# Kernel tuning notes

Measured on AMD Instinct MI355X. Metric: run time of the kernel, lower is better.

## Reference

```python
import jax, jax.numpy as jnp
import numpy as np

B, S, D, H, DFF = 4, 1024, 1024, 16, 4096
DK = D // H
EPS = 1e-9


def _layernorm(x, alpha, bias):
    # Faithful to source: torch.std is unbiased (ddof=1), eps added to std.
    mean = jnp.mean(x, axis=-1, keepdims=True)
    xc = x - mean
    std = jnp.sqrt(jnp.sum(xc * xc, axis=-1, keepdims=True) / (x.shape[-1] - 1))
    return alpha * xc / (std + EPS) + bias


def _mha(x, wq_w, wq_b, wo_w, wo_b):
    # Source bug preserved: w_q is used for q, k, AND v projections.
    p = (x @ wq_w + wq_b).reshape(B, S, H, DK).transpose(0, 2, 1, 3)  # [B,H,S,DK]
    scores = jnp.einsum('bhqd,bhkd->bhqk', p, p) / jnp.sqrt(jnp.asarray(DK, x.dtype))
    attn = jax.nn.softmax(scores, axis=-1)
    out = jnp.einsum('bhqk,bhkd->bhqd', attn, p)
    out = out.transpose(0, 2, 1, 3).reshape(B, S, D)
    return out @ wo_w + wo_b


def _ffn(x, w1, b1, w2, b2):
    return jax.nn.relu(x @ w1 + b1) @ w2 + b2


def setup_inputs() -> dict:
    key = jax.random.key(0)
    ks = jax.random.split(key, 8)
    sc = 0.02
    return {
        'x': jax.random.normal(ks[0], (B, S, D), jnp.float32),
        'wq_w': sc * jax.random.normal(ks[1], (D, D), jnp.float32),
        'wq_b': jnp.zeros((D,), jnp.float32),
        'wo_w': sc * jax.random.normal(ks[2], (D, D), jnp.float32),
        'wo_b': jnp.zeros((D,), jnp.float32),
        'ff1_w': sc * jax.random.normal(ks[3], (D, DFF), jnp.float32),
        'ff1_b': jnp.zeros((DFF,), jnp.float32),
        'ff2_w': sc * jax.random.normal(ks[4], (DFF, D), jnp.float32),
        'ff2_b': jnp.zeros((D,), jnp.float32),
        'alpha1': jnp.ones((1,), jnp.float32), 'bias1': jnp.zeros((1,), jnp.float32),
        'alpha2': jnp.ones((1,), jnp.float32), 'bias2': jnp.zeros((1,), jnp.float32),
        'alpha3': jnp.ones((1,), jnp.float32), 'bias3': jnp.zeros((1,), jnp.float32),
    }


def reference(x, wq_w, wq_b, wo_w, wo_b, ff1_w, ff1_b, ff2_w, ff2_b,
              alpha1, bias1, alpha2, bias2, alpha3, bias3):
    h1 = x + _mha(_layernorm(x, alpha1, bias1), wq_w, wq_b, wo_w, wo_b)
    h2 = h1 + _ffn(_layernorm(h1, alpha2, bias2), ff1_w, ff1_b, ff2_w, ff2_b)
    return _layernorm(h2, alpha3, bias3)
```

## Files before the change

kernel.cpp:

```cpp
#include <hip/hip_runtime.h>

typedef short short8 __attribute__((ext_vector_type(8)));
typedef float f32x4 __attribute__((ext_vector_type(4)));
typedef unsigned short u16x4 __attribute__((ext_vector_type(4)));

#define DEV static __device__ __forceinline__

DEV float b2f(unsigned short u) { return __uint_as_float(((unsigned)u) << 16); }
DEV unsigned short f2b(float f) {
    unsigned u = __float_as_uint(f);
    u += 0x7FFFu + ((u >> 16) & 1u);
    return (unsigned short)(u >> 16);
}
DEV float wred_sum(float v) {
#pragma unroll
    for (int o = 32; o; o >>= 1) v += __shfl_xor(v, o);
    return v;
}

DEV void gld_lds16(const unsigned short* g, unsigned short* l) {
    __builtin_amdgcn_global_load_lds((const __attribute__((address_space(1))) void*)g,
                                     (__attribute__((address_space(3))) void*)l, 16, 0, 0);
}

template <bool OUT_BF16>
__global__ __launch_bounds__(256) void ln_kernel(const float* __restrict__ in,
                                                 void* __restrict__ out_v,
                                                 const float* __restrict__ alpha_p,
                                                 const float* __restrict__ bias_p) {
    __shared__ float redA[4], redB[4];
    const int row = blockIdx.x;
    const int t = threadIdx.x;
    const int lane = t & 63, w = t >> 6;

    f32x4 xv = *(const f32x4*)&in[(size_t)row * 1024 + t * 4];

    float s = wred_sum(xv[0] + xv[1] + xv[2] + xv[3]);
    if (lane == 0) redA[w] = s;
    __syncthreads();
    float mean = (redA[0] + redA[1] + redA[2] + redA[3]) * (1.0f / 1024.0f);

    float d0 = xv[0] - mean, d1 = xv[1] - mean, d2 = xv[2] - mean, d3 = xv[3] - mean;
    float ss = wred_sum(d0 * d0 + d1 * d1 + d2 * d2 + d3 * d3);
    if (lane == 0) redB[w] = ss;
    __syncthreads();
    float var = (redB[0] + redB[1] + redB[2] + redB[3]) * (1.0f / 1023.0f);
    float denom = sqrtf(var) + 1e-9f;
    float inv = alpha_p[0] / denom;
    float bias = bias_p[0];

    if (OUT_BF16) {
        u16x4 o;
        o[0] = f2b(d0 * inv + bias);
        o[1] = f2b(d1 * inv + bias);
        o[2] = f2b(d2 * inv + bias);
        o[3] = f2b(d3 * inv + bias);
        *(u16x4*)&((unsigned short*)out_v)[(size_t)row * 1024 + t * 4] = o;
    } else {
        f32x4 o;
        o[0] = d0 * inv + bias;
        o[1] = d1 * inv + bias;
        o[2] = d2 * inv + bias;
        o[3] = d3 * inv + bias;
        *(f32x4*)&((float*)out_v)[(size_t)row * 1024 + t * 4] = o;
    }
}

__global__ __launch_bounds__(256) void transpose_cast_kernel(const float* __restrict__ in,
                                                             unsigned short* __restrict__ out,
                                                             int R, int C) {
    __shared__ unsigned short tile[32][33];
    const int c0 = blockIdx.x * 32, r0 = blockIdx.y * 32;
    const int x = threadIdx.x, y0 = threadIdx.y;
#pragma unroll
    for (int yy = y0; yy < 32; yy += 8) tile[yy][x] = f2b(in[(size_t)(r0 + yy) * C + c0 + x]);
    __syncthreads();
#pragma unroll
    for (int yy = y0; yy < 32; yy += 8) out[(size_t)(c0 + yy) * R + r0 + x] = tile[x][yy];
}

__global__ __launch_bounds__(256) void transpose_bf16_batch(const unsigned short* __restrict__ in,
                                                            unsigned short* __restrict__ out) {
    __shared__ unsigned short tile[32][33];
    const int b = blockIdx.z;
    const int d0 = blockIdx.x * 32, s0 = blockIdx.y * 32;
    const unsigned short* I = in + (size_t)b * 1024 * 1024;
    unsigned short* O = out + (size_t)b * 1024 * 1024;
    const int x = threadIdx.x, y0 = threadIdx.y;
#pragma unroll
    for (int yy = y0; yy < 32; yy += 8) tile[yy][x] = I[(size_t)(s0 + yy) * 1024 + d0 + x];
    __syncthreads();
#pragma unroll
    for (int yy = y0; yy < 32; yy += 8) O[(size_t)(d0 + yy) * 1024 + s0 + x] = tile[x][yy];
}

template <int BM, int BN, bool RELU, bool RES, bool OUT_BF16>
__global__ __launch_bounds__(256) void gemm2(const unsigned short* __restrict__ A,
                                             const unsigned short* __restrict__ Bt,
                                             const float* __restrict__ bias,
                                             const float* __restrict__ res,
                                             void* __restrict__ C_v,
                                             int M, int N, int K) {
    constexpr int WM = BM / 2, WN = BN / 2;
    constexpr int FM = WM / 16, FN = WN / 16;
    __shared__ __align__(16) unsigned short As[BM * 64];
    __shared__ __align__(16) unsigned short Bs[BN * 64];

    const int t = threadIdx.x;
    const int lane = t & 63, w = t >> 6;
    const int wr = w >> 1, wc = w & 1;
    const int lr = lane & 15, g = lane >> 4;

    const int nwg = gridDim.x;
    const int cpx = nwg >> 3;
    const int wg = blockIdx.x;
    const int swz = (wg & 7) * cpx + (wg >> 3);
    const int NB = N / BN;
    const int m0 = (swz / NB) * BM, n0 = (swz % NB) * BN;

    f32x4 acc[FM][FN];
#pragma unroll
    for (int i = 0; i < FM; ++i)
#pragma unroll
        for (int j = 0; j < FN; ++j) acc[i][j] = (f32x4)0.0f;

    for (int k0 = 0; k0 < K; k0 += 64) {
        __syncthreads();
#pragma unroll
        for (int i = 0; i < BM / 32; ++i) {
            int id = i * 256 + t;
            int row = id >> 3, ch = id & 7;
            gld_lds16(&A[(size_t)(m0 + row) * K + k0 + ((ch ^ (row & 7)) * 8)],
                      &As[(size_t)(i * 256 + (t & ~63)) * 8]);
        }
#pragma unroll
        for (int i = 0; i < BN / 32; ++i) {
            int id = i * 256 + t;
            int row = id >> 3, ch = id & 7;
            gld_lds16(&Bt[(size_t)(n0 + row) * K + k0 + ((ch ^ (row & 7)) * 8)],
                      &Bs[(size_t)(i * 256 + (t & ~63)) * 8]);
        }
        __syncthreads();

        short8 af[FM][2], bfr[FN][2];
#pragma unroll
        for (int mi = 0; mi < FM; ++mi) {
            int row = wr * WM + mi * 16 + lr;
#pragma unroll
            for (int ks = 0; ks < 2; ++ks) {
                int ch = (ks * 4 + g) ^ (row & 7);
                af[mi][ks] = *(const short8*)&As[row * 64 + ch * 8];
            }
        }
#pragma unroll
        for (int ni = 0; ni < FN; ++ni) {
            int row = wc * WN + ni * 16 + lr;
#pragma unroll
            for (int ks = 0; ks < 2; ++ks) {
                int ch = (ks * 4 + g) ^ (row & 7);
                bfr[ni][ks] = *(const short8*)&Bs[row * 64 + ch * 8];
            }
        }
#pragma unroll
        for (int ks = 0; ks < 2; ++ks)
#pragma unroll
            for (int mi = 0; mi < FM; ++mi)
#pragma unroll
                for (int ni = 0; ni < FN; ++ni)
                    acc[mi][ni] = __builtin_amdgcn_mfma_f32_16x16x32_bf16(af[mi][ks], bfr[ni][ks], acc[mi][ni], 0, 0, 0);
    }

    const int lg = g;
#pragma unroll
    for (int ni = 0; ni < FN; ++ni) {
        int col = n0 + wc * WN + ni * 16 + lr;
        float bv = bias[col];
#pragma unroll
        for (int mi = 0; mi < FM; ++mi) {
            int row0 = m0 + wr * WM + mi * 16 + lg * 4;
#pragma unroll
            for (int i = 0; i < 4; ++i) {
                int row = row0 + i;
                float x = acc[mi][ni][i] + bv;
                if (RES) x += res[(size_t)row * N + col];
                if (RELU) x = fmaxf(x, 0.0f);
                if (OUT_BF16)
                    ((unsigned short*)C_v)[(size_t)row * N + col] = f2b(x);
                else
                    ((float*)C_v)[(size_t)row * N + col] = x;
            }
        }
    }
}

__global__ __launch_bounds__(256) void attn_mfma_kernel(const unsigned short* __restrict__ p,
                                                        const unsigned short* __restrict__ pT,
                                                        unsigned short* __restrict__ out) {
    __shared__ __align__(16) unsigned short Ks[64 * 64];
    __shared__ __align__(16) unsigned short Vt[64 * 64];
    __shared__ __align__(16) unsigned short Ps[4 * 16 * 64];

    const int t = threadIdx.x;
    const int lane = t & 63, w = t >> 6;
    const int lr = lane & 15, g = lane >> 4;
    const int qblk = blockIdx.x;
    const int bh = blockIdx.y;
    const int b = bh >> 4, h = bh & 15;

    const unsigned short* Pm = p + (size_t)b * (1024 * 1024) + h * 64;
    const unsigned short* PT = pT + (size_t)b * (1024 * 1024) + (size_t)(h * 64) * 1024;

    const int q0 = qblk * 64 + w * 16;
    short8 qa0 = *(const short8*)&Pm[(size_t)(q0 + lr) * 1024 + g * 8];
    short8 qa1 = *(const short8*)&Pm[(size_t)(q0 + lr) * 1024 + 32 + g * 8];

    f32x4 acc[4];
#pragma unroll
    for (int i = 0; i < 4; ++i) acc[i] = (f32x4)0.0f;
    float mrow[4] = {-1e30f, -1e30f, -1e30f, -1e30f};
    float lsum[4] = {0.f, 0.f, 0.f, 0.f};

    unsigned short* Pw = &Ps[w * 16 * 64];

    for (int kt = 0; kt < 16; ++kt) {
        const int key0 = kt * 64;
        __syncthreads();
#pragma unroll
        for (int i = 0; i < 2; ++i) {
            int id = t + i * 256;
            int row = id >> 3, ch = (id & 7) * 8;
            int sw = ch ^ ((row & 7) << 3);
            short8 kv = *(const short8*)&Pm[(size_t)(key0 + row) * 1024 + ch];
            *(short8*)&Ks[row * 64 + sw] = kv;
            short8 vv = *(const short8*)&PT[(size_t)row * 1024 + key0 + ch];
            *(short8*)&Vt[row * 64 + sw] = vv;
        }
        __syncthreads();

        f32x4 s_acc[4];
#pragma unroll
        for (int kg = 0; kg < 4; ++kg) {
            s_acc[kg] = (f32x4)0.0f;
            int krow = kg * 16 + lr;
            int swz = (krow & 7) << 3;
            short8 kb0 = *(const short8*)&Ks[krow * 64 + ((g * 8) ^ swz)];
            short8 kb1 = *(const short8*)&Ks[krow * 64 + ((32 + g * 8) ^ swz)];
            s_acc[kg] = __builtin_amdgcn_mfma_f32_16x16x32_bf16(qa0, kb0, s_acc[kg], 0, 0, 0);
            s_acc[kg] = __builtin_amdgcn_mfma_f32_16x16x32_bf16(qa1, kb1, s_acc[kg], 0, 0, 0);
        }

#pragma unroll
        for (int reg = 0; reg < 4; ++reg) {
            float mx = fmaxf(fmaxf(s_acc[0][reg], s_acc[1][reg]),
                             fmaxf(s_acc[2][reg], s_acc[3][reg])) * 0.125f;
            mx = fmaxf(mx, __shfl_xor(mx, 1));
            mx = fmaxf(mx, __shfl_xor(mx, 2));
            mx = fmaxf(mx, __shfl_xor(mx, 4));
            mx = fmaxf(mx, __shfl_xor(mx, 8));
            float mnew = fmaxf(mrow[reg], mx);
            float scale = __expf(mrow[reg] - mnew);
            mrow[reg] = mnew;
            float psum = 0.f;
#pragma unroll
            for (int kg = 0; kg < 4; ++kg) {
                float pv = __expf(s_acc[kg][reg] * 0.125f - mnew);
                s_acc[kg][reg] = pv;
                psum += pv;
            }
            psum += __shfl_xor(psum, 1);
            psum += __shfl_xor(psum, 2);
            psum += __shfl_xor(psum, 4);
            psum += __shfl_xor(psum, 8);
            lsum[reg] = lsum[reg] * scale + psum;
#pragma unroll
            for (int dg = 0; dg < 4; ++dg) acc[dg][reg] *= scale;
        }

#pragma unroll
        for (int reg = 0; reg < 4; ++reg) {
            int q = g * 4 + reg;
            int swz = (q & 7) << 3;
#pragma unroll
            for (int kg = 0; kg < 4; ++kg) {
                int key = lr + 16 * kg;
                Pw[q * 64 + (key ^ swz)] = f2b(s_acc[kg][reg]);
            }
        }
        int pswz = (lr & 7) << 3;
        short8 pa0 = *(const short8*)&Pw[lr * 64 + ((g * 8) ^ pswz)];
        short8 pa1 = *(const short8*)&Pw[lr * 64 + ((32 + g * 8) ^ pswz)];

#pragma unroll
        for (int dg = 0; dg < 4; ++dg) {
            int drow = dg * 16 + lr;
            int swz = (drow & 7) << 3;
            short8 vb0 = *(const short8*)&Vt[drow * 64 + ((g * 8) ^ swz)];
            short8 vb1 = *(const short8*)&Vt[drow * 64 + ((32 + g * 8) ^ swz)];
            acc[dg] = __builtin_amdgcn_mfma_f32_16x16x32_bf16(pa0, vb0, acc[dg], 0, 0, 0);
            acc[dg] = __builtin_amdgcn_mfma_f32_16x16x32_bf16(pa1, vb1, acc[dg], 0, 0, 0);
        }
    }

    unsigned short* O = out + (size_t)b * (1024 * 1024) + h * 64;
#pragma unroll
    for (int reg = 0; reg < 4; ++reg) {
        float inv = 1.0f / lsum[reg];
        int q = q0 + g * 4 + reg;
#pragma unroll
        for (int dg = 0; dg < 4; ++dg) {
            O[(size_t)q * 1024 + dg * 16 + lr] = f2b(acc[dg][reg] * inv);
        }
    }
}

extern "C" void kernel_launch(void* const* d_in, const int* in_sizes, int n_in,
                              void* d_out, int out_size, void* d_ws, size_t ws_size,
                              hipStream_t stream) {
    const float* x = (const float*)d_in[0];
    const float* wq_w = (const float*)d_in[1];
    const float* wq_b = (const float*)d_in[2];
    const float* wo_w = (const float*)d_in[3];
    const float* wo_b = (const float*)d_in[4];
    const float* ff1_w = (const float*)d_in[5];
    const float* ff1_b = (const float*)d_in[6];
    const float* ff2_w = (const float*)d_in[7];
    const float* ff2_b = (const float*)d_in[8];
    const float* alpha1 = (const float*)d_in[9];
    const float* bias1 = (const float*)d_in[10];
    const float* alpha2 = (const float*)d_in[11];
    const float* bias2 = (const float*)d_in[12];
    const float* alpha3 = (const float*)d_in[13];
    const float* bias3 = (const float*)d_in[14];
    float* out = (float*)d_out;

    const size_t MB = 1u << 20;
    char* ws = (char*)d_ws;
    unsigned short* wq_t = (unsigned short*)(ws + 0 * MB);
    unsigned short* wo_t = (unsigned short*)(ws + 2 * MB);
    unsigned short* ff1_t = (unsigned short*)(ws + 4 * MB);
    unsigned short* ff2_t = (unsigned short*)(ws + 12 * MB);
    unsigned short* lnbuf = (unsigned short*)(ws + 20 * MB);
    unsigned short* pbuf = (unsigned short*)(ws + 28 * MB);
    unsigned short* attn = (unsigned short*)(ws + 36 * MB);
    float* h1 = (float*)(ws + 44 * MB);
    unsigned short* pbT = (unsigned short*)(ws + 60 * MB);
    unsigned short* mid = (unsigned short*)(ws + 60 * MB);
    float* h2 = (float*)(ws + 28 * MB);

    const int M = 4096;

    transpose_cast_kernel<<<dim3(32, 32), dim3(32, 8), 0, stream>>>(wq_w, wq_t, 1024, 1024);
    transpose_cast_kernel<<<dim3(32, 32), dim3(32, 8), 0, stream>>>(wo_w, wo_t, 1024, 1024);
    transpose_cast_kernel<<<dim3(128, 32), dim3(32, 8), 0, stream>>>(ff1_w, ff1_t, 1024, 4096);
    transpose_cast_kernel<<<dim3(32, 128), dim3(32, 8), 0, stream>>>(ff2_w, ff2_t, 4096, 1024);

    ln_kernel<true><<<M, 256, 0, stream>>>(x, lnbuf, alpha1, bias1);
    gemm2<128, 64, false, false, true><<<512, 256, 0, stream>>>(lnbuf, wq_t, wq_b, nullptr, pbuf, M, 1024, 1024);
    transpose_bf16_batch<<<dim3(32, 32, 4), dim3(32, 8), 0, stream>>>(pbuf, pbT);
    attn_mfma_kernel<<<dim3(16, 64), 256, 0, stream>>>(pbuf, pbT, attn);
    gemm2<128, 64, false, true, false><<<512, 256, 0, stream>>>(attn, wo_t, wo_b, x, h1, M, 1024, 1024);
    ln_kernel<true><<<M, 256, 0, stream>>>(h1, lnbuf, alpha2, bias2);
    gemm2<128, 128, true, false, true><<<1024, 256, 0, stream>>>(lnbuf, ff1_t, ff1_b, nullptr, mid, M, 4096, 1024);
    gemm2<128, 64, false, true, false><<<512, 256, 0, stream>>>(mid, ff2_t, ff2_b, h1, h2, M, 1024, 4096);
    ln_kernel<false><<<M, 256, 0, stream>>>(h2, out, alpha3, bias3);
}
```

Before: 258.8 us.

## Double-buffer attention K/V tiles via async LDS loads and skip softmax rescale

The attention kernel now double-buffers the K and V^T tiles in LDS, loading them with global_load_lds directly into shared memory, with the source address swizzled so the LDS layout keeps the XOR pattern. The next tile is prefetched while the current one is computed, leaving one barrier per iteration. It also raises wave priority around the MFMA blocks and skips the online-softmax rescale when the new row max exceeds the running max by at most 8, a lazy-rescale trick that stays exact because the final division normalises. The grid is reordered so blocks sharing a head are spread differently, which could change L2 reuse. Attention is only part of the whole layer, so the overall effect is limited.

```diff
diff --git a/kernel.cpp b/kernel.cpp
--- a/kernel.cpp
+++ b/kernel.cpp
@@ -193,18 +193,18 @@
     }
 }
 
-__global__ __launch_bounds__(256) void attn_mfma_kernel(const unsigned short* __restrict__ p,
-                                                        const unsigned short* __restrict__ pT,
-                                                        unsigned short* __restrict__ out) {
-    __shared__ __align__(16) unsigned short Ks[64 * 64];
-    __shared__ __align__(16) unsigned short Vt[64 * 64];
+__global__ __launch_bounds__(256) void attn_mfma2(const unsigned short* __restrict__ p,
+                                                  const unsigned short* __restrict__ pT,
+                                                  unsigned short* __restrict__ out) {
+    __shared__ __align__(16) unsigned short Ks[2][64 * 64];
+    __shared__ __align__(16) unsigned short Vt[2][64 * 64];
     __shared__ __align__(16) unsigned short Ps[4 * 16 * 64];
 
     const int t = threadIdx.x;
     const int lane = t & 63, w = t >> 6;
     const int lr = lane & 15, g = lane >> 4;
-    const int qblk = blockIdx.x;
-    const int bh = blockIdx.y;
+    const int bh = blockIdx.x;
+    const int qblk = blockIdx.y;
     const int b = bh >> 4, h = bh & 15;
 
     const unsigned short* Pm = p + (size_t)b * (1024 * 1024) + h * 64;
@@ -222,58 +222,90 @@
 
     unsigned short* Pw = &Ps[w * 16 * 64];
 
+#define STAGE(buf, kt)                                                                     \
+    {                                                                                      \
+        const int key0 = (kt) * 64;                                                        \
+        _Pragma("unroll") for (int i = 0; i < 2; ++i) {                                    \
+            int id = i * 256 + t;                                                          \
+            int row = id >> 3, ch = id & 7;                                                \
+            gld_lds16(&Pm[(size_t)(key0 + row) * 1024 + ((ch ^ (row & 7)) * 8)],           \
+                      &Ks[buf][(size_t)(i * 256 + (t & ~63)) * 8]);                        \
+            gld_lds16(&PT[(size_t)row * 1024 + key0 + ((ch ^ (row & 7)) * 8)],             \
+                      &Vt[buf][(size_t)(i * 256 + (t & ~63)) * 8]);                        \
+        }                                                                                  \
+    }
+
+    STAGE(0, 0);
+    __syncthreads();
+    int cur = 0;
+
     for (int kt = 0; kt < 16; ++kt) {
-        const int key0 = kt * 64;
-        __syncthreads();
-#pragma unroll
-        for (int i = 0; i < 2; ++i) {
-            int id = t + i * 256;
-            int row = id >> 3, ch = (id & 7) * 8;
-            int sw = ch ^ ((row & 7) << 3);
-            short8 kv = *(const short8*)&Pm[(size_t)(key0 + row) * 1024 + ch];
-            *(short8*)&Ks[row * 64 + sw] = kv;
-            short8 vv = *(const short8*)&PT[(size_t)row * 1024 + key0 + ch];
-            *(short8*)&Vt[row * 64 + sw] = vv;
-        }
-        __syncthreads();
+        if (kt < 15) STAGE(cur ^ 1, kt + 1);
 
         f32x4 s_acc[4];
+        __builtin_amdgcn_s_setprio(1);
 #pragma unroll
         for (int kg = 0; kg < 4; ++kg) {
             s_acc[kg] = (f32x4)0.0f;
             int krow = kg * 16 + lr;
             int swz = (krow & 7) << 3;
-            short8 kb0 = *(const short8*)&Ks[krow * 64 + ((g * 8) ^ swz)];
-            short8 kb1 = *(const short8*)&Ks[krow * 64 + ((32 + g * 8) ^ swz)];
+            short8 kb0 = *(const short8*)&Ks[cur][krow * 64 + ((g * 8) ^ swz)];
+            short8 kb1 = *(const short8*)&Ks[cur][krow * 64 + ((32 + g * 8) ^ swz)];
             s_acc[kg] = __builtin_amdgcn_mfma_f32_16x16x32_bf16(qa0, kb0, s_acc[kg], 0, 0, 0);
             s_acc[kg] = __builtin_amdgcn_mfma_f32_16x16x32_bf16(qa1, kb1, s_acc[kg], 0, 0, 0);
         }
-
+        __builtin_amdgcn_s_setprio(0);
+
+        float mx[4];
 #pragma unroll
         for (int reg = 0; reg < 4; ++reg) {
-            float mx = fmaxf(fmaxf(s_acc[0][reg], s_acc[1][reg]),
-                             fmaxf(s_acc[2][reg], s_acc[3][reg])) * 0.125f;
-            mx = fmaxf(mx, __shfl_xor(mx, 1));
-            mx = fmaxf(mx, __shfl_xor(mx, 2));
-            mx = fmaxf(mx, __shfl_xor(mx, 4));
-            mx = fmaxf(mx, __shfl_xor(mx, 8));
-            float mnew = fmaxf(mrow[reg], mx);
-            float scale = __expf(mrow[reg] - mnew);
-            mrow[reg] = mnew;
-            float psum = 0.f;
-#pragma unroll
-            for (int kg = 0; kg < 4; ++kg) {
-                float pv = __expf(s_acc[kg][reg] * 0.125f - mnew);
-                s_acc[kg][reg] = pv;
-                psum += pv;
-            }
-            psum += __shfl_xor(psum, 1);
-            psum += __shfl_xor(psum, 2);
-            psum += __shfl_xor(psum, 4);
-            psum += __shfl_xor(psum, 8);
-            lsum[reg] = lsum[reg] * scale + psum;
-#pragma unroll
-            for (int dg = 0; dg < 4; ++dg) acc[dg][reg] *= scale;
+            float m = fmaxf(fmaxf(s_acc[0][reg], s_acc[1][reg]),
+                            fmaxf(s_acc[2][reg], s_acc[3][reg])) * 0.125f;
+            m = fmaxf(m, __shfl_xor(m, 1));
+            m = fmaxf(m, __shfl_xor(m, 2));
+            m = fmaxf(m, __shfl_xor(m, 4));
+            m = fmaxf(m, __shfl_xor(m, 8));
+            mx[reg] = m;
+        }
+        bool small = (mx[0] <= mrow[0] + 8.f) && (mx[1] <= mrow[1] + 8.f) &&
+                     (mx[2] <= mrow[2] + 8.f) && (mx[3] <= mrow[3] + 8.f);
+        if (__all(small)) {
+#pragma unroll
+            for (int reg = 0; reg < 4; ++reg) {
+                float psum = 0.f;
+#pragma unroll
+                for (int kg = 0; kg < 4; ++kg) {
+                    float pv = __expf(s_acc[kg][reg] * 0.125f - mrow[reg]);
+                    s_acc[kg][reg] = pv;
+                    psum += pv;
+                }
+                psum += __shfl_xor(psum, 1);
+                psum += __shfl_xor(psum, 2);
+                psum += __shfl_xor(psum, 4);
+                psum += __shfl_xor(psum, 8);
+                lsum[reg] += psum;
+            }
+        } else {
+#pragma unroll
+            for (int reg = 0; reg < 4; ++reg) {
+                float mnew = fmaxf(mrow[reg], mx[reg]);
+                float scale = __expf(mrow[reg] - mnew);
+                mrow[reg] = mnew;
+                float psum = 0.f;
+#pragma unroll
+                for (int kg = 0; kg < 4; ++kg) {
+                    float pv = __expf(s_acc[kg][reg] * 0.125f - mnew);
+                    s_acc[kg][reg] = pv;
+                    psum += pv;
+                }
+                psum += __shfl_xor(psum, 1);
+                psum += __shfl_xor(psum, 2);
+                psum += __shfl_xor(psum, 4);
+                psum += __shfl_xor(psum, 8);
+                lsum[reg] = lsum[reg] * scale + psum;
+#pragma unroll
+                for (int dg = 0; dg < 4; ++dg) acc[dg][reg] *= scale;
+            }
         }
 
 #pragma unroll
@@ -290,16 +322,22 @@
         short8 pa0 = *(const short8*)&Pw[lr * 64 + ((g * 8) ^ pswz)];
         short8 pa1 = *(const short8*)&Pw[lr * 64 + ((32 + g * 8) ^ pswz)];
 
+        __builtin_amdgcn_s_setprio(1);
 #pragma unroll
         for (int dg = 0; dg < 4; ++dg) {
             int drow = dg * 16 + lr;
             int swz = (drow & 7) << 3;
-            short8 vb0 = *(const short8*)&Vt[drow * 64 + ((g * 8) ^ swz)];
-            short8 vb1 = *(const short8*)&Vt[drow * 64 + ((32 + g * 8) ^ swz)];
+            short8 vb0 = *(const short8*)&Vt[cur][drow * 64 + ((g * 8) ^ swz)];
+            short8 vb1 = *(const short8*)&Vt[cur][drow * 64 + ((32 + g * 8) ^ swz)];
             acc[dg] = __builtin_amdgcn_mfma_f32_16x16x32_bf16(pa0, vb0, acc[dg], 0, 0, 0);
             acc[dg] = __builtin_amdgcn_mfma_f32_16x16x32_bf16(pa1, vb1, acc[dg], 0, 0, 0);
         }
-    }
+        __builtin_amdgcn_s_setprio(0);
+
+        __syncthreads();
+        cur ^= 1;
+    }
+#undef STAGE
 
     unsigned short* O = out + (size_t)b * (1024 * 1024) + h * 64;
 #pragma unroll
@@ -357,7 +395,7 @@
     ln_kernel<true><<<M, 256, 0, stream>>>(x, lnbuf, alpha1, bias1);
     gemm2<128, 64, false, false, true><<<512, 256, 0, stream>>>(lnbuf, wq_t, wq_b, nullptr, pbuf, M, 1024, 1024);
     transpose_bf16_batch<<<dim3(32, 32, 4), dim3(32, 8), 0, stream>>>(pbuf, pbT);
-    attn_mfma_kernel<<<dim3(16, 64), 256, 0, stream>>>(pbuf, pbT, attn);
+    attn_mfma2<<<dim3(64, 16), 256, 0, stream>>>(pbuf, pbT, attn);
     gemm2<128, 64, false, true, false><<<512, 256, 0, stream>>>(attn, wo_t, wo_b, x, h1, M, 1024, 1024);
     ln_kernel<true><<<M, 256, 0, stream>>>(h1, lnbuf, alpha2, bias2);
     gemm2<128, 128, true, false, true><<<1024, 256, 0, stream>>>(lnbuf, ff1_t, ff1_b, nullptr, mid, M, 4096, 1024);
```

Result: slower. 270.3 us (+4.5%).

## Rewrite attention with 32x32 MFMA, register P exchange, and deferred softmax rescale

Applied to the files above, without the earlier changes.

Replaces the 16x16 MFMA flash-attention kernel with one built on 32x32x16 MFMAs. It computes S^T so each lane owns a query column, and reads K/V straight from global memory (L2) instead of staging them in LDS behind block barriers. The P tile is repacked into bf16 MFMA operands through cross-lane shuffles rather than a round trip through LDS. Softmax uses exp2 with a threshold-deferred max update, so rescaling is skipped while the running max stays within bounds. Risks include heavier global/L2 traffic from repeated K/V reads without LDS reuse, and a new grid shape (64x8 blocks of 128 queries).

```diff
diff --git a/kernel.cpp b/kernel.cpp
--- a/kernel.cpp
+++ b/kernel.cpp
@@ -2,7 +2,9 @@
 
 typedef short short8 __attribute__((ext_vector_type(8)));
 typedef float f32x4 __attribute__((ext_vector_type(4)));
+typedef float f32x16 __attribute__((ext_vector_type(16)));
 typedef unsigned short u16x4 __attribute__((ext_vector_type(4)));
+typedef unsigned uint4v __attribute__((ext_vector_type(4)));
 
 #define DEV static __device__ __forceinline__
 
@@ -12,11 +14,15 @@
     u += 0x7FFFu + ((u >> 16) & 1u);
     return (unsigned short)(u >> 16);
 }
+DEV unsigned pack2(float a, float b) {
+    return (unsigned)f2b(a) | ((unsigned)f2b(b) << 16);
+}
 DEV float wred_sum(float v) {
 #pragma unroll
     for (int o = 32; o; o >>= 1) v += __shfl_xor(v, o);
     return v;
 }
+DEV float fast_exp2(float x) { return __builtin_exp2f(x); }
 
 DEV void gld_lds16(const unsigned short* g, unsigned short* l) {
     __builtin_amdgcn_global_load_lds((const __attribute__((address_space(1))) void*)g,
@@ -193,123 +199,132 @@
     }
 }
 
-__global__ __launch_bounds__(256) void attn_mfma_kernel(const unsigned short* __restrict__ p,
-                                                        const unsigned short* __restrict__ pT,
-                                                        unsigned short* __restrict__ out) {
-    __shared__ __align__(16) unsigned short Ks[64 * 64];
-    __shared__ __align__(16) unsigned short Vt[64 * 64];
-    __shared__ __align__(16) unsigned short Ps[4 * 16 * 64];
+__global__ __launch_bounds__(256) void attn_mfma5(const unsigned short* __restrict__ p,
+                                                  const unsigned short* __restrict__ pT,
+                                                  unsigned short* __restrict__ out) {
+    __shared__ float Olds[4][32][65];
 
     const int t = threadIdx.x;
     const int lane = t & 63, w = t >> 6;
-    const int lr = lane & 15, g = lane >> 4;
-    const int qblk = blockIdx.x;
-    const int bh = blockIdx.y;
+    const int ql = lane & 31, hi = lane >> 5;
+    const int bh = blockIdx.x;
+    const int qt = blockIdx.y;
     const int b = bh >> 4, h = bh & 15;
 
     const unsigned short* Pm = p + (size_t)b * (1024 * 1024) + h * 64;
     const unsigned short* PT = pT + (size_t)b * (1024 * 1024) + (size_t)(h * 64) * 1024;
 
-    const int q0 = qblk * 64 + w * 16;
-    short8 qa0 = *(const short8*)&Pm[(size_t)(q0 + lr) * 1024 + g * 8];
-    short8 qa1 = *(const short8*)&Pm[(size_t)(q0 + lr) * 1024 + 32 + g * 8];
-
-    f32x4 acc[4];
-#pragma unroll
-    for (int i = 0; i < 4; ++i) acc[i] = (f32x4)0.0f;
-    float mrow[4] = {-1e30f, -1e30f, -1e30f, -1e30f};
-    float lsum[4] = {0.f, 0.f, 0.f, 0.f};
-
-    unsigned short* Pw = &Ps[w * 16 * 64];
-
-    for (int kt = 0; kt < 16; ++kt) {
-        const int key0 = kt * 64;
-        __syncthreads();
-#pragma unroll
-        for (int i = 0; i < 2; ++i) {
-            int id = t + i * 256;
-            int row = id >> 3, ch = (id & 7) * 8;
-            int sw = ch ^ ((row & 7) << 3);
-            short8 kv = *(const short8*)&Pm[(size_t)(key0 + row) * 1024 + ch];
-            *(short8*)&Ks[row * 64 + sw] = kv;
-            short8 vv = *(const short8*)&PT[(size_t)row * 1024 + key0 + ch];
-            *(short8*)&Vt[row * 64 + sw] = vv;
-        }
-        __syncthreads();
-
-        f32x4 s_acc[4];
-#pragma unroll
-        for (int kg = 0; kg < 4; ++kg) {
-            s_acc[kg] = (f32x4)0.0f;
-            int krow = kg * 16 + lr;
-            int swz = (krow & 7) << 3;
-            short8 kb0 = *(const short8*)&Ks[krow * 64 + ((g * 8) ^ swz)];
-            short8 kb1 = *(const short8*)&Ks[krow * 64 + ((32 + g * 8) ^ swz)];
-            s_acc[kg] = __builtin_amdgcn_mfma_f32_16x16x32_bf16(qa0, kb0, s_acc[kg], 0, 0, 0);
-            s_acc[kg] = __builtin_amdgcn_mfma_f32_16x16x32_bf16(qa1, kb1, s_acc[kg], 0, 0, 0);
-        }
-
-#pragma unroll
-        for (int reg = 0; reg < 4; ++reg) {
-            float mx = fmaxf(fmaxf(s_acc[0][reg], s_acc[1][reg]),
-                             fmaxf(s_acc[2][reg], s_acc[3][reg])) * 0.125f;
-            mx = fmaxf(mx, __shfl_xor(mx, 1));
-            mx = fmaxf(mx, __shfl_xor(mx, 2));
-            mx = fmaxf(mx, __shfl_xor(mx, 4));
-            mx = fmaxf(mx, __shfl_xor(mx, 8));
-            float mnew = fmaxf(mrow[reg], mx);
-            float scale = __expf(mrow[reg] - mnew);
-            mrow[reg] = mnew;
-            float psum = 0.f;
-#pragma unroll
-            for (int kg = 0; kg < 4; ++kg) {
-                float pv = __expf(s_acc[kg][reg] * 0.125f - mnew);
-                s_acc[kg][reg] = pv;
-                psum += pv;
-            }
-            psum += __shfl_xor(psum, 1);
-            psum += __shfl_xor(psum, 2);
-            psum += __shfl_xor(psum, 4);
-            psum += __shfl_xor(psum, 8);
-            lsum[reg] = lsum[reg] * scale + psum;
-#pragma unroll
-            for (int dg = 0; dg < 4; ++dg) acc[dg][reg] *= scale;
-        }
-
-#pragma unroll
-        for (int reg = 0; reg < 4; ++reg) {
-            int q = g * 4 + reg;
-            int swz = (q & 7) << 3;
-#pragma unroll
-            for (int kg = 0; kg < 4; ++kg) {
-                int key = lr + 16 * kg;
-                Pw[q * 64 + (key ^ swz)] = f2b(s_acc[kg][reg]);
-            }
-        }
-        int pswz = (lr & 7) << 3;
-        short8 pa0 = *(const short8*)&Pw[lr * 64 + ((g * 8) ^ pswz)];
-        short8 pa1 = *(const short8*)&Pw[lr * 64 + ((32 + g * 8) ^ pswz)];
-
-#pragma unroll
-        for (int dg = 0; dg < 4; ++dg) {
-            int drow = dg * 16 + lr;
-            int swz = (drow & 7) << 3;
-            short8 vb0 = *(const short8*)&Vt[drow * 64 + ((g * 8) ^ swz)];
-            short8 vb1 = *(const short8*)&Vt[drow * 64 + ((32 + g * 8) ^ swz)];
-            acc[dg] = __builtin_amdgcn_mfma_f32_16x16x32_bf16(pa0, vb0, acc[dg], 0, 0, 0);
-            acc[dg] = __builtin_amdgcn_mfma_f32_16x16x32_bf16(pa1, vb1, acc[dg], 0, 0, 0);
-        }
-    }
-
+    const int q0 = qt * 128 + w * 32;
+
+    short8 qb[4];
+#pragma unroll
+    for (int s = 0; s < 4; ++s)
+        qb[s] = *(const short8*)&Pm[(size_t)(q0 + ql) * 1024 + 16 * s + 8 * hi];
+
+    f32x16 oacc0 = (f32x16)0.0f, oacc1 = (f32x16)0.0f;
+    float mrow = -1e30f;
+    float lsum = 0.0f;
+
+    const float C2 = 0.18033688011112042f;
+    const float THR2 = 11.541560327111708f;
+
+    for (int step = 0; step < 32; ++step) {
+        const int key0 = step * 32;
+
+        f32x16 sacc = (f32x16)0.0f;
+#pragma unroll
+        for (int s = 0; s < 4; ++s) {
+            short8 ka = *(const short8*)&Pm[(size_t)(key0 + ql) * 1024 + 16 * s + 8 * hi];
+            sacc = __builtin_amdgcn_mfma_f32_32x32x16_bf16(ka, qb[s], sacc, 0, 0, 0);
+        }
+
+        short8 va00 = *(const short8*)&PT[(size_t)ql * 1024 + key0 + 8 * hi];
+        short8 va01 = *(const short8*)&PT[(size_t)ql * 1024 + key0 + 16 + 8 * hi];
+        short8 va10 = *(const short8*)&PT[(size_t)(32 + ql) * 1024 + key0 + 8 * hi];
+        short8 va11 = *(const short8*)&PT[(size_t)(32 + ql) * 1024 + key0 + 16 + 8 * hi];
+
+        float m01 = fmaxf(sacc[0], sacc[1]), m23 = fmaxf(sacc[2], sacc[3]);
+        float m45 = fmaxf(sacc[4], sacc[5]), m67 = fmaxf(sacc[6], sacc[7]);
+        float m89 = fmaxf(sacc[8], sacc[9]), mab = fmaxf(sacc[10], sacc[11]);
+        float mcd = fmaxf(sacc[12], sacc[13]), mef = fmaxf(sacc[14], sacc[15]);
+        float mx = fmaxf(fmaxf(fmaxf(m01, m23), fmaxf(m45, m67)),
+                         fmaxf(fmaxf(m89, mab), fmaxf(mcd, mef)));
+        mx = fmaxf(mx, __shfl_xor(mx, 32));
+        float mx2 = mx * C2;
+
+        float pf[16];
+        bool defer = (mx2 <= mrow + THR2);
+        if (__all(defer)) {
+#pragma unroll
+            for (int r = 0; r < 16; ++r) pf[r] = fast_exp2(fmaf(sacc[r], C2, -mrow));
+        } else {
+            float mnew = fmaxf(mrow, mx2);
+            float scale = fast_exp2(mrow - mnew);
+            mrow = mnew;
+#pragma unroll
+            for (int r = 0; r < 16; ++r) pf[r] = fast_exp2(fmaf(sacc[r], C2, -mnew));
+            lsum *= scale;
+#pragma unroll
+            for (int r = 0; r < 16; ++r) { oacc0[r] *= scale; oacc1[r] *= scale; }
+        }
+        float ps = ((pf[0] + pf[1]) + (pf[2] + pf[3])) + ((pf[4] + pf[5]) + (pf[6] + pf[7])) +
+                   (((pf[8] + pf[9]) + (pf[10] + pf[11])) + ((pf[12] + pf[13]) + (pf[14] + pf[15])));
+        lsum += ps;
+
+        unsigned wd0 = pack2(pf[0], pf[1]), wd1 = pack2(pf[2], pf[3]);
+        unsigned wd2 = pack2(pf[4], pf[5]), wd3 = pack2(pf[6], pf[7]);
+        unsigned wd4 = pack2(pf[8], pf[9]), wd5 = pack2(pf[10], pf[11]);
+        unsigned wd6 = pack2(pf[12], pf[13]), wd7 = pack2(pf[14], pf[15]);
+
+        unsigned x0 = (unsigned)__shfl_xor((int)wd0, 32);
+        unsigned x1 = (unsigned)__shfl_xor((int)wd1, 32);
+        unsigned x2 = (unsigned)__shfl_xor((int)wd2, 32);
+        unsigned x3 = (unsigned)__shfl_xor((int)wd3, 32);
+        unsigned x4 = (unsigned)__shfl_xor((int)wd4, 32);
+        unsigned x5 = (unsigned)__shfl_xor((int)wd5, 32);
+        unsigned x6 = (unsigned)__shfl_xor((int)wd6, 32);
+        unsigned x7 = (unsigned)__shfl_xor((int)wd7, 32);
+
+        union U8 { unsigned u[4]; short8 s; };
+        U8 pb0, pb1;
+        pb0.u[0] = hi ? x2 : wd0;
+        pb0.u[1] = hi ? x3 : wd1;
+        pb0.u[2] = hi ? wd2 : x0;
+        pb0.u[3] = hi ? wd3 : x1;
+        pb1.u[0] = hi ? x6 : wd4;
+        pb1.u[1] = hi ? x7 : wd5;
+        pb1.u[2] = hi ? wd6 : x4;
+        pb1.u[3] = hi ? wd7 : x5;
+
+        oacc0 = __builtin_amdgcn_mfma_f32_32x32x16_bf16(va00, pb0.s, oacc0, 0, 0, 0);
+        oacc0 = __builtin_amdgcn_mfma_f32_32x32x16_bf16(va01, pb1.s, oacc0, 0, 0, 0);
+        oacc1 = __builtin_amdgcn_mfma_f32_32x32x16_bf16(va10, pb0.s, oacc1, 0, 0, 0);
+        oacc1 = __builtin_amdgcn_mfma_f32_32x32x16_bf16(va11, pb1.s, oacc1, 0, 0, 0);
+    }
+
+    lsum += __shfl_xor(lsum, 32);
+    float inv = 1.0f / lsum;
+
+#pragma unroll
+    for (int r = 0; r < 16; ++r) {
+        int d = (r & 3) + 8 * (r >> 2) + 4 * hi;
+        Olds[w][ql][d] = oacc0[r] * inv;
+        Olds[w][ql][32 + d] = oacc1[r] * inv;
+    }
     unsigned short* O = out + (size_t)b * (1024 * 1024) + h * 64;
-#pragma unroll
-    for (int reg = 0; reg < 4; ++reg) {
-        float inv = 1.0f / lsum[reg];
-        int q = q0 + g * 4 + reg;
-#pragma unroll
-        for (int dg = 0; dg < 4; ++dg) {
-            O[(size_t)q * 1024 + dg * 16 + lr] = f2b(acc[dg][reg] * inv);
-        }
+    unsigned wo[16];
+#pragma unroll
+    for (int j = 0; j < 16; ++j) {
+        float a = Olds[w][ql][hi * 32 + 2 * j];
+        float c = Olds[w][ql][hi * 32 + 2 * j + 1];
+        wo[j] = pack2(a, c);
+    }
+    uint4v* dst = (uint4v*)&O[(size_t)(q0 + ql) * 1024 + hi * 32];
+#pragma unroll
+    for (int j = 0; j < 4; ++j) {
+        uint4v v;
+        v[0] = wo[4 * j]; v[1] = wo[4 * j + 1]; v[2] = wo[4 * j + 2]; v[3] = wo[4 * j + 3];
+        dst[j] = v;
     }
 }
 
@@ -357,7 +372,7 @@
     ln_kernel<true><<<M, 256, 0, stream>>>(x, lnbuf, alpha1, bias1);
     gemm2<128, 64, false, false, true><<<512, 256, 0, stream>>>(lnbuf, wq_t, wq_b, nullptr, pbuf, M, 1024, 1024);
     transpose_bf16_batch<<<dim3(32, 32, 4), dim3(32, 8), 0, stream>>>(pbuf, pbT);
-    attn_mfma_kernel<<<dim3(16, 64), 256, 0, stream>>>(pbuf, pbT, attn);
+    attn_mfma5<<<dim3(64, 8), 256, 0, stream>>>(pbuf, pbT, attn);
     gemm2<128, 64, false, true, false><<<512, 256, 0, stream>>>(attn, wo_t, wo_b, x, h1, M, 1024, 1024);
     ln_kernel<true><<<M, 256, 0, stream>>>(h1, lnbuf, alpha2, bias2);
     gemm2<128, 128, true, false, true><<<1024, 256, 0, stream>>>(lnbuf, ff1_t, ff1_b, nullptr, mid, M, 4096, 1024);
```

Result: slower. 264.2 us (+2.1%).
